# Optimization experiments

Measured on AMD Instinct MI355X. Metric: run time of the kernel, lower is better.

## Reference

```python
import jax, jax.numpy as jnp
import numpy as np

N_QUBITS = 10
DEPTH = 2
FEATURES = 64
HIDDEN = 512
NUM_HIDDEN_LAYERS = 2
BATCH = 32768
DIM = 2 ** N_QUBITS
LOG2PI = float(np.log(2.0 * np.pi))


def _cx_perm(c, t, n):
    # CNOT(control=c, target=t) as a basis permutation (qiskit little-endian bits)
    j = np.arange(2 ** n)
    return j ^ (((j >> c) & 1) << t)

_CX_PERMS = [_cx_perm(q, q + 1, N_QUBITS) for q in range(N_QUBITS - 1)] + [_cx_perm(N_QUBITS - 1, 0, N_QUBITS)]
# Z-expectation sign table: signs[i, j] = +1 if bit i of j is 0 else -1
_SIGNS = np.stack([1.0 - 2.0 * ((np.arange(DIM) >> i) & 1) for i in range(N_QUBITS)]).astype(np.float32)


def _apply_1q(state, gate, q):
    # state: [B, 2^n] complex64; gate: [2,2] (shared) or [B,2,2] (per-sample)
    hi = DIM // (2 ** (q + 1))
    lo = 2 ** q
    s = state.reshape(-1, hi, 2, lo)
    if gate.ndim == 2:
        out = jnp.einsum('ij,bhjl->bhil', gate, s)
    else:
        out = jnp.einsum('bij,bhjl->bhil', gate, s)
    return out.reshape(state.shape)


def _rot_gate(kind, th):
    c = jnp.cos(th / 2).astype(jnp.complex64)
    s = jnp.sin(th / 2).astype(jnp.complex64)
    if kind == 'rx':
        return jnp.stack([jnp.stack([c, -1j * s]), jnp.stack([-1j * s, c])])
    if kind == 'ry':
        return jnp.stack([jnp.stack([c, -s]), jnp.stack([s, c])])
    thc = th.astype(jnp.complex64)
    em = jnp.exp(-0.5j * thc)
    ep = jnp.exp(0.5j * thc)
    z = jnp.zeros((), jnp.complex64)
    return jnp.stack([jnp.stack([em, z]), jnp.stack([z, ep])])


def quantum_expectations(xq, theta):
    # Batched statevector simulation of QuantumLayer circuit. xq: [B, n_qubits]
    B = xq.shape[0]
    state = jnp.zeros((B, DIM), jnp.complex64).at[:, 0].set(1.0)
    # data-encoding RY(2*arctan(x_i)) per qubit (per-sample angle)
    for q in range(N_QUBITS):
        th = 2.0 * jnp.arctan(xq[:, q])
        c = jnp.cos(th / 2).astype(jnp.complex64)
        s = jnp.sin(th / 2).astype(jnp.complex64)
        g = jnp.stack([jnp.stack([c, -s], -1), jnp.stack([s, c], -1)], -2)  # [B,2,2]
        state = _apply_1q(state, g, q)
    idx = 0
    for _ in range(DEPTH):
        for q in range(N_QUBITS):
            state = _apply_1q(state, _rot_gate('rx', theta[idx]), q); idx += 1
            state = _apply_1q(state, _rot_gate('ry', theta[idx]), q); idx += 1
            state = _apply_1q(state, _rot_gate('rz', theta[idx]), q); idx += 1
        for perm in _CX_PERMS:
            state = state[:, perm]
    probs = jnp.abs(state) ** 2  # [B, 2^n]
    return probs @ jnp.asarray(_SIGNS).T  # [B, n_qubits] <Z_i> expectations


def ar_net(x, W_in, b_in, W_h, b_h, W_out, b_out):
    # NOTE: original forward never applies the registered masks -> plain dense MLP
    h = jnp.tanh(x @ W_in.T + b_in)
    for l in range(NUM_HIDDEN_LAYERS):
        h = jnp.tanh(h @ W_h[l].T + b_h[l])
    out = h @ W_out.T + b_out
    shift, log_scale = jnp.split(out, 2, axis=-1)
    return shift, jnp.exp(log_scale)


def setup_inputs() -> dict:
    key = jax.random.key(0)
    ks = jax.random.split(key, 8)

    def lin_w(k, fo, fi):
        b = 1.0 / np.sqrt(fi)
        return jax.random.uniform(k, (fo, fi), jnp.float32, -b, b)

    x = jax.random.normal(ks[0], (BATCH, FEATURES), jnp.float32)
    theta = jax.random.normal(ks[1], (3 * N_QUBITS * DEPTH,), jnp.float32) * 0.01
    W_in = lin_w(ks[2], HIDDEN, FEATURES)
    b_in = jax.random.uniform(ks[3], (HIDDEN,), jnp.float32, -1.0 / np.sqrt(FEATURES), 1.0 / np.sqrt(FEATURES))
    W_h = jnp.stack([lin_w(jax.random.fold_in(ks[4], l), HIDDEN, HIDDEN) for l in range(NUM_HIDDEN_LAYERS)])
    b_h = jax.random.uniform(ks[5], (NUM_HIDDEN_LAYERS, HIDDEN), jnp.float32, -1.0 / np.sqrt(HIDDEN), 1.0 / np.sqrt(HIDDEN))
    W_out = lin_w(ks[6], 2 * FEATURES, HIDDEN)
    b_out = jax.random.uniform(ks[7], (2 * FEATURES,), jnp.float32, -1.0 / np.sqrt(HIDDEN), 1.0 / np.sqrt(HIDDEN))
    return {"x": x, "theta": theta, "W_in": W_in, "b_in": b_in, "W_h": W_h, "b_h": b_h, "W_out": W_out, "b_out": b_out}


def reference(x, theta, W_in, b_in, W_h, b_h, W_out, b_out):
    q = quantum_expectations(x[:, :N_QUBITS], theta)  # [B, n_qubits]
    q = jax.lax.stop_gradient(q)  # torch detaches via torch.tensor(numpy)
    enhanced = jnp.concatenate([q, x[:, N_QUBITS:]], axis=1)  # [B, FEATURES]
    shift, scale = ar_net(enhanced, W_in, b_in, W_h, b_h, W_out, b_out)
    z = (enhanced - shift) / scale
    log_det = -jnp.sum(jnp.log(scale), axis=1)
    log_prob = jnp.sum(-0.5 * z ** 2 - 0.5 * LOG2PI, axis=1) + log_det
    return log_prob
```

## Files before the change

kernel.cpp:

```cpp
#include <hip/hip_runtime.h>
#include <hip/hip_bf16.h>
#include <math.h>


#define N_SAMPLES 32768
#define FEAT 64

typedef unsigned short u16;
typedef __attribute__((ext_vector_type(2))) float f32x2;
typedef __attribute__((ext_vector_type(8))) short bf16x8_t;
typedef __attribute__((ext_vector_type(4))) float f32x4_t;

__device__ __forceinline__ u16 f2bf(float v) {
    __hip_bfloat16 b = __float2bfloat16(v);
    return __builtin_bit_cast(u16, b);
}
__device__ __forceinline__ float bf2f(u16 u) {
    return __bfloat162float(__builtin_bit_cast(__hip_bfloat16, u));
}

__device__ __forceinline__ f32x2 cmul(f32x2 a, f32x2 b) {
    f32x2 r = (f32x2){a.x, a.x} * b;
    f32x2 bs = __builtin_shufflevector(b, b, 1, 0);
    r = (f32x2){-a.y, a.y} * bs + r;
    return r;
}
template<int M>
__device__ __forceinline__ float xexf(float v) {
    if constexpr (M < 32) {
        constexpr int pat = (M << 10) | 0x1f;
        return __uint_as_float(__builtin_amdgcn_ds_swizzle(__float_as_uint(v), pat));
    } else {
        return __shfl_xor(v, 32, 64);
    }
}
template<int M>
__device__ __forceinline__ f32x2 xex2(f32x2 v) {
    return (f32x2){xexf<M>(v.x), xexf<M>(v.y)};
}

template<int Q>
__device__ __forceinline__ void rot_gate(f32x2 (&amp)[16],
                                         f32x2 g00, f32x2 g01, f32x2 g10, f32x2 g11,
                                         int lane) {
    if constexpr (Q < 4) {
        #pragma unroll
        for (int t = 0; t < 16; ++t) {
            if ((t & (1 << Q)) == 0) {
                const int t1 = t | (1 << Q);
                f32x2 a = amp[t], b = amp[t1];
                amp[t]  = cmul(g00, a) + cmul(g01, b);
                amp[t1] = cmul(g10, a) + cmul(g11, b);
            }
        }
    } else {
        constexpr int xm = 1 << (Q - 4);
        const bool hi = (lane >> (Q - 4)) & 1;
        f32x2 ga = hi ? g11 : g00;
        f32x2 gb = hi ? g10 : g01;
        #pragma unroll
        for (int t = 0; t < 16; ++t) {
            f32x2 b = xex2<xm>(amp[t]);
            amp[t] = cmul(ga, amp[t]) + cmul(gb, b);
        }
    }
}

template<int C, int T>
__device__ __forceinline__ void cx_local(f32x2 (&amp)[16]) {
    #pragma unroll
    for (int t = 0; t < 16; ++t) {
        if (((t >> C) & 1) && !((t >> T) & 1)) {
            const int t1 = t | (1 << T);
            f32x2 tmp = amp[t]; amp[t] = amp[t1]; amp[t1] = tmp;
        }
    }
}
__device__ __forceinline__ void cx_3_4(f32x2 (&amp)[16]) {
    #pragma unroll
    for (int t = 0; t < 16; ++t)
        if ((t >> 3) & 1) amp[t] = xex2<1>(amp[t]);
}
template<int CL, int TL>
__device__ __forceinline__ void cx_lane(f32x2 (&amp)[16], int lane) {
    const bool ctrl = (lane >> CL) & 1;
    #pragma unroll
    for (int t = 0; t < 16; ++t) {
        f32x2 v = xex2<(1 << TL)>(amp[t]);
        if (ctrl) amp[t] = v;
    }
}
__device__ __forceinline__ void cx_9_0(f32x2 (&amp)[16], int lane) {
    const bool ctrl = (lane >> 5) & 1;
    #pragma unroll
    for (int t = 0; t < 16; t += 2) {
        f32x2 a = amp[t], b = amp[t + 1];
        amp[t]     = ctrl ? b : a;
        amp[t + 1] = ctrl ? a : b;
    }
}

__global__ __launch_bounds__(256)
void qkernel(const float* __restrict__ x, const float* __restrict__ theta,
             float* __restrict__ enh) {
    __shared__ f32x2 gbuf[20][4];
    const int tid = threadIdx.x;
    if (tid < 20) {
        const int base = tid * 3;
        float s1, c1, s2, c2, sz, cz;
        sincosf(0.5f * theta[base + 0], &s1, &c1);
        sincosf(0.5f * theta[base + 1], &s2, &c2);
        sincosf(0.5f * theta[base + 2], &sz, &cz);
        f32x2 m00 = (f32x2){ c2*c1,  s2*s1};
        f32x2 m01 = (f32x2){-s2*c1, -c2*s1};
        f32x2 m10 = (f32x2){ s2*c1, -c2*s1};
        f32x2 m11 = (f32x2){ c2*c1, -s2*s1};
        f32x2 e0 = (f32x2){cz, -sz}, e1 = (f32x2){cz, sz};
        gbuf[tid][0] = cmul(e0, m00);
        gbuf[tid][1] = cmul(e0, m01);
        gbuf[tid][2] = cmul(e1, m10);
        gbuf[tid][3] = cmul(e1, m11);
    }
    __syncthreads();

    const int lane = tid & 63;
    const int s = blockIdx.x * 4 + (tid >> 6);
    const float xr = x[s * FEAT + lane];

    const float inv = 1.0f / sqrtf(fmaf(xr, xr, 1.0f));
    const float cq = inv, sq = xr * inv;

    float csv[10], snv[10];
    #pragma unroll
    for (int i = 0; i < 10; ++i) {
        csv[i] = __shfl(cq, i, 64);
        snv[i] = __shfl(sq, i, 64);
    }

    float lf = ((lane >> 0) & 1) ? snv[4] : csv[4];
    lf *= ((lane >> 1) & 1) ? snv[5] : csv[5];
    lf *= ((lane >> 2) & 1) ? snv[6] : csv[6];
    lf *= ((lane >> 3) & 1) ? snv[7] : csv[7];
    lf *= ((lane >> 4) & 1) ? snv[8] : csv[8];
    lf *= ((lane >> 5) & 1) ? snv[9] : csv[9];
    float l01[4], l23[4];
    l01[0] = csv[0]*csv[1]; l01[1] = snv[0]*csv[1];
    l01[2] = csv[0]*snv[1]; l01[3] = snv[0]*snv[1];
    l23[0] = csv[2]*csv[3]; l23[1] = snv[2]*csv[3];
    l23[2] = csv[2]*snv[3]; l23[3] = snv[2]*snv[3];

    f32x2 amp[16];
    #pragma unroll
    for (int t = 0; t < 16; ++t)
        amp[t] = (f32x2){lf * l01[t & 3] * l23[(t >> 2) & 3], 0.f};

    #pragma unroll
    for (int l = 0; l < 2; ++l) {
        const f32x2* gl = &gbuf[l * 10][0];
        #define ROT(Q) rot_gate<Q>(amp, gl[Q*4+0], gl[Q*4+1], gl[Q*4+2], gl[Q*4+3], lane);
        ROT(0) ROT(1) ROT(2) ROT(3) ROT(4) ROT(5) ROT(6) ROT(7) ROT(8) ROT(9)
        #undef ROT
        cx_local<0,1>(amp); cx_local<1,2>(amp); cx_local<2,3>(amp);
        cx_3_4(amp);
        cx_lane<0,1>(amp, lane); cx_lane<1,2>(amp, lane); cx_lane<2,3>(amp, lane);
        cx_lane<3,4>(amp, lane); cx_lane<4,5>(amp, lane);
        cx_9_0(amp, lane);
    }

    float p[16];
    #pragma unroll
    for (int t = 0; t < 16; ++t) p[t] = amp[t].x*amp[t].x + amp[t].y*amp[t].y;
    float o[10];
    #pragma unroll
    for (int i = 0; i < 4; ++i) {
        float acc = 0.f;
        #pragma unroll
        for (int t = 0; t < 16; ++t) acc += ((t >> i) & 1) ? -p[t] : p[t];
        o[i] = acc;
    }
    float ptot = 0.f;
    #pragma unroll
    for (int t = 0; t < 16; ++t) ptot += p[t];
    #pragma unroll
    for (int i = 4; i < 10; ++i) o[i] = ((lane >> (i - 4)) & 1) ? -ptot : ptot;
    #pragma unroll
    for (int i = 0; i < 10; ++i) {
        #pragma unroll
        for (int b = 1; b < 64; b <<= 1) o[i] += __shfl_xor(o[i], b, 64);
    }
    float outv = xr;
    #pragma unroll
    for (int i = 0; i < 10; ++i) if (lane == i) outv = o[i];
    enh[s * FEAT + lane] = outv;
}

__global__ __launch_bounds__(256)
void prep(const float* __restrict__ W_in, const float* __restrict__ W_h,
          const float* __restrict__ W_out,
          u16* __restrict__ win_hi, u16* __restrict__ win_lo,
          u16* __restrict__ wh_hi,  u16* __restrict__ wh_lo,
          u16* __restrict__ wout_hi,u16* __restrict__ wout_lo) {
    const int i = blockIdx.x * 256 + threadIdx.x;
    float v; u16 *ph, *pl; int off;
    if (i < 32768)        { v = W_in[i];          ph = win_hi;  pl = win_lo;  off = i; }
    else if (i < 557056)  { off = i - 32768;  v = W_h[off];   ph = wh_hi;   pl = wh_lo;  }
    else                  { off = i - 557056; v = W_out[off]; ph = wout_hi; pl = wout_lo; }
    const u16 hi = f2bf(v);
    const u16 lo = f2bf(v - bf2f(hi));
    ph[off] = hi; pl[off] = lo;
}

__device__ __forceinline__ float fast_tanh(float x) {
    const float e = __expf(2.0f * x);
    return 1.0f - 2.0f * __builtin_amdgcn_rcpf(e + 1.0f);
}

#define MT 4

template<int K, int NT>
__device__ __forceinline__ void gemm_frag(
        const u16* __restrict__ Whi, const u16* __restrict__ Wlo,
        const u16* hHi, const u16* hLo, int lane, int colbase,
        f32x4_t (&acc)[MT][NT]) {
    constexpr int KS = K / 32;
    const int l15 = lane & 15, l4 = lane >> 4, l7 = lane & 7;

    #pragma unroll
    for (int mt = 0; mt < MT; ++mt)
        #pragma unroll
        for (int nt = 0; nt < NT; ++nt) acc[mt][nt] = (f32x4_t)0.f;

    int woff[NT];
    #pragma unroll
    for (int nt = 0; nt < NT; ++nt)
        woff[nt] = (colbase + nt * 16 + l15) * K + l4 * 8;

    bf16x8_t pH[NT], pL[NT], qH[NT], qL[NT];
    #pragma unroll
    for (int nt = 0; nt < NT; ++nt) {
        pH[nt] = *(const bf16x8_t*)&Whi[woff[nt]];
        pL[nt] = *(const bf16x8_t*)&Wlo[woff[nt]];
        qH[nt] = *(const bf16x8_t*)&Whi[woff[nt] + 32];
        qL[nt] = *(const bf16x8_t*)&Wlo[woff[nt] + 32];
    }

    int ks = 0;
    #pragma unroll 1
    for (; ks + 2 < KS; ks += 2) {
        {
            bf16x8_t aH[MT], aL[MT];
            #pragma unroll
            for (int mt = 0; mt < MT; ++mt) {
                const int m = mt * 16 + l15;
                const int off = m * K + (((ks * 4 + l4) ^ (m & 7)) * 8);
                aH[mt] = *(const bf16x8_t*)&hHi[off];
                aL[mt] = *(const bf16x8_t*)&hLo[off];
            }
            #pragma unroll
            for (int nt = 0; nt < NT; ++nt)
                #pragma unroll
                for (int mt = 0; mt < MT; ++mt) {
                    acc[mt][nt] = __builtin_amdgcn_mfma_f32_16x16x32_bf16(aH[mt], pH[nt], acc[mt][nt], 0, 0, 0);
                    acc[mt][nt] = __builtin_amdgcn_mfma_f32_16x16x32_bf16(aH[mt], pL[nt], acc[mt][nt], 0, 0, 0);
                    acc[mt][nt] = __builtin_amdgcn_mfma_f32_16x16x32_bf16(aL[mt], pH[nt], acc[mt][nt], 0, 0, 0);
                }
        }
        #pragma unroll
        for (int nt = 0; nt < NT; ++nt) {
            pH[nt] = *(const bf16x8_t*)&Whi[woff[nt] + (ks + 2) * 32];
            pL[nt] = *(const bf16x8_t*)&Wlo[woff[nt] + (ks + 2) * 32];
        }
        {
            bf16x8_t aH[MT], aL[MT];
            #pragma unroll
            for (int mt = 0; mt < MT; ++mt) {
                const int m = mt * 16 + l15;
                const int off = m * K + ((((ks + 1) * 4 + l4) ^ (m & 7)) * 8);
                aH[mt] = *(const bf16x8_t*)&hHi[off];
                aL[mt] = *(const bf16x8_t*)&hLo[off];
            }
            #pragma unroll
            for (int nt = 0; nt < NT; ++nt)
                #pragma unroll
                for (int mt = 0; mt < MT; ++mt) {
                    acc[mt][nt] = __builtin_amdgcn_mfma_f32_16x16x32_bf16(aH[mt], qH[nt], acc[mt][nt], 0, 0, 0);
                    acc[mt][nt] = __builtin_amdgcn_mfma_f32_16x16x32_bf16(aH[mt], qL[nt], acc[mt][nt], 0, 0, 0);
                    acc[mt][nt] = __builtin_amdgcn_mfma_f32_16x16x32_bf16(aL[mt], qH[nt], acc[mt][nt], 0, 0, 0);
                }
        }
        #pragma unroll
        for (int nt = 0; nt < NT; ++nt) {
            qH[nt] = *(const bf16x8_t*)&Whi[woff[nt] + (ks + 3) * 32];
            qL[nt] = *(const bf16x8_t*)&Wlo[woff[nt] + (ks + 3) * 32];
        }
    }
    {
        bf16x8_t aH[MT], aL[MT];
        #pragma unroll
        for (int mt = 0; mt < MT; ++mt) {
            const int m = mt * 16 + l15;
            const int off = m * K + (((ks * 4 + l4) ^ (m & 7)) * 8);
            aH[mt] = *(const bf16x8_t*)&hHi[off];
            aL[mt] = *(const bf16x8_t*)&hLo[off];
        }
        #pragma unroll
        for (int nt = 0; nt < NT; ++nt)
            #pragma unroll
            for (int mt = 0; mt < MT; ++mt) {
                acc[mt][nt] = __builtin_amdgcn_mfma_f32_16x16x32_bf16(aH[mt], pH[nt], acc[mt][nt], 0, 0, 0);
                acc[mt][nt] = __builtin_amdgcn_mfma_f32_16x16x32_bf16(aH[mt], pL[nt], acc[mt][nt], 0, 0, 0);
                acc[mt][nt] = __builtin_amdgcn_mfma_f32_16x16x32_bf16(aL[mt], pH[nt], acc[mt][nt], 0, 0, 0);
            }
        #pragma unroll
        for (int mt = 0; mt < MT; ++mt) {
            const int m = mt * 16 + l15;
            const int off = m * K + ((((ks + 1) * 4 + l4) ^ (m & 7)) * 8);
            aH[mt] = *(const bf16x8_t*)&hHi[off];
            aL[mt] = *(const bf16x8_t*)&hLo[off];
        }
        #pragma unroll
        for (int nt = 0; nt < NT; ++nt)
            #pragma unroll
            for (int mt = 0; mt < MT; ++mt) {
                acc[mt][nt] = __builtin_amdgcn_mfma_f32_16x16x32_bf16(aH[mt], qH[nt], acc[mt][nt], 0, 0, 0);
                acc[mt][nt] = __builtin_amdgcn_mfma_f32_16x16x32_bf16(aH[mt], qL[nt], acc[mt][nt], 0, 0, 0);
                acc[mt][nt] = __builtin_amdgcn_mfma_f32_16x16x32_bf16(aL[mt], qH[nt], acc[mt][nt], 0, 0, 0);
            }
    }
}

template<int NT>
__device__ __forceinline__ void write_h(
        f32x4_t (&acc)[MT][NT], const float* __restrict__ bias,
        u16* hHi, u16* hLo, int lane, int colbase) {
    const int l15 = lane & 15, l4 = lane >> 4;
    #pragma unroll
    for (int nt = 0; nt < NT; ++nt) {
        const int n = colbase + nt * 16 + l15;
        const float b = bias[n];
        #pragma unroll
        for (int mt = 0; mt < MT; ++mt)
            #pragma unroll
            for (int r = 0; r < 4; ++r) {
                const int m = mt * 16 + l4 * 4 + r;
                const float v = fast_tanh(acc[mt][nt][r] + b);
                const u16 hi = f2bf(v);
                const u16 lo = f2bf(v - bf2f(hi));
                const int blk = (n >> 3) ^ (m & 7);
                const int off = m * 512 + blk * 8 + (n & 7);
                hHi[off] = hi; hLo[off] = lo;
            }
    }
}

__global__ __attribute__((amdgpu_waves_per_eu(2, 2))) __launch_bounds__(512)
void mlpkernel(const float* __restrict__ enh,
               const u16* __restrict__ win_hi, const u16* __restrict__ win_lo,
               const float* __restrict__ b_in,
               const u16* __restrict__ wh_hi,  const u16* __restrict__ wh_lo,
               const float* __restrict__ b_h,
               const u16* __restrict__ wout_hi,const u16* __restrict__ wout_lo,
               const float* __restrict__ b_out,
               float* __restrict__ out) {
    __shared__ u16 hHi[64 * 512];
    __shared__ u16 hLo[64 * 512];
    const int tid = threadIdx.x;
    const int lane = tid & 63, w = tid >> 6;
    const int row0 = blockIdx.x * 64;

    {
        const int r = tid >> 3, c0 = (tid & 7) * 8;
        const float4 v0 = *(const float4*)&enh[(row0 + r) * FEAT + c0];
        const float4 v1 = *(const float4*)&enh[(row0 + r) * FEAT + c0 + 4];
        const float vv[8] = {v0.x, v0.y, v0.z, v0.w, v1.x, v1.y, v1.z, v1.w};
        bf16x8_t vh, vl;
        #pragma unroll
        for (int j = 0; j < 8; ++j) {
            const u16 hi = f2bf(vv[j]);
            const u16 lo = f2bf(vv[j] - bf2f(hi));
            vh[j] = (short)hi; vl[j] = (short)lo;
        }
        const int off = r * 64 + (((c0 >> 3) ^ (r & 7)) * 8);
        *(bf16x8_t*)&hHi[off] = vh;
        *(bf16x8_t*)&hLo[off] = vl;
    }
    __syncthreads();

    f32x4_t acc[MT][4];
    gemm_frag<64, 4>(win_hi, win_lo, hHi, hLo, lane, w * 64, acc);
    __syncthreads();
    write_h<4>(acc, b_in, hHi, hLo, lane, w * 64);
    __syncthreads();
    gemm_frag<512, 4>(wh_hi, wh_lo, hHi, hLo, lane, w * 64, acc);
    __syncthreads();
    write_h<4>(acc, b_h, hHi, hLo, lane, w * 64);
    __syncthreads();
    gemm_frag<512, 4>(wh_hi + 262144, wh_lo + 262144, hHi, hLo, lane, w * 64, acc);
    __syncthreads();
    write_h<4>(acc, b_h + 512, hHi, hLo, lane, w * 64);
    __syncthreads();
    f32x4_t acc2[MT][1];
    gemm_frag<512, 1>(wout_hi, wout_lo, hHi, hLo, lane, w * 16, acc2);
    __syncthreads();

    float* f = (float*)hHi;
    {
        const int l15 = lane & 15, l4 = lane >> 4;
        const int n = w * 16 + l15;
        const float b = b_out[n];
        #pragma unroll
        for (int mt = 0; mt < MT; ++mt)
            #pragma unroll
            for (int r = 0; r < 4; ++r) {
                const int m = mt * 16 + l4 * 4 + r;
                f[m * 128 + n] = acc2[mt][0][r] + b;
            }
    }
    __syncthreads();

    const float HALF_LOG2PI = 0.9189385332046727f;
    #pragma unroll
    for (int rr = 0; rr < 8; ++rr) {
        const int row = w * 8 + rr;
        const float shift = f[row * 128 + lane];
        const float ls    = f[row * 128 + 64 + lane];
        const float e     = enh[(row0 + row) * FEAT + lane];
        const float z = (e - shift) * __expf(-ls);
        float term = fmaf(-0.5f * z, z, -HALF_LOG2PI) - ls;
        #pragma unroll
        for (int b = 1; b < 64; b <<= 1) term += __shfl_xor(term, b, 64);
        if (lane == 0) out[row0 + row] = term;
    }
}

extern "C" void kernel_launch(void* const* d_in, const int* in_sizes, int n_in,
                              void* d_out, int out_size, void* d_ws, size_t ws_size,
                              hipStream_t stream) {
    const float* x     = (const float*)d_in[0];
    const float* theta = (const float*)d_in[1];
    const float* W_in  = (const float*)d_in[2];
    const float* b_in  = (const float*)d_in[3];
    const float* W_h   = (const float*)d_in[4];
    const float* b_h   = (const float*)d_in[5];
    const float* W_out = (const float*)d_in[6];
    const float* b_out = (const float*)d_in[7];
    float* out = (float*)d_out;

    float* enh = (float*)d_ws;
    u16* wbuf = (u16*)((char*)d_ws + (size_t)N_SAMPLES * FEAT * 4);
    u16* win_hi  = wbuf;
    u16* win_lo  = win_hi + 32768;
    u16* wh_hi   = win_lo + 32768;
    u16* wh_lo   = wh_hi + 524288;
    u16* wout_hi = wh_lo + 524288;
    u16* wout_lo = wout_hi + 65536;

    qkernel<<<dim3(N_SAMPLES / 4), dim3(256), 0, stream>>>(x, theta, enh);
    prep<<<dim3(2432), dim3(256), 0, stream>>>(W_in, W_h, W_out,
        win_hi, win_lo, wh_hi, wh_lo, wout_hi, wout_lo);
    mlpkernel<<<dim3(N_SAMPLES / 64), dim3(512), 0, stream>>>(
        enh, win_hi, win_lo, b_in, wh_hi, wh_lo, b_h, wout_hi, wout_lo, b_out, out);
}
```

Before: 438.3 us.

## Fold second-layer CNOT ring into rotated bases and merge quantum/prep kernels

Absorbs the trailing CNOT permutations into the second layer's rotation gates by applying each gate in a transformed basis, using parity-based partner indices and gate selection. The Z expectations are then read from parity sums with lane-dependent sign flips, and the first layer's CNOTs are dropped as separate shuffles. The weight-splitting prep kernel is merged into the quantum kernel launch as extra blocks, removing one launch. The MLP kernel's waves_per_eu lower bound is relaxed from 2 to 1, and the basis-mapping derivation is intricate, so an error would affect correctness.

```diff
diff --git a/kernel.cpp b/kernel.cpp
--- a/kernel.cpp
+++ b/kernel.cpp
@@ -5,6 +5,8 @@
 
 #define N_SAMPLES 32768
 #define FEAT 64
+#define QBLOCKS (N_SAMPLES / 4)
+#define PREPBLOCKS 2432
 
 typedef unsigned short u16;
 typedef __attribute__((ext_vector_type(2))) float f32x2;
@@ -27,11 +29,13 @@
 }
 template<int M>
 __device__ __forceinline__ float xexf(float v) {
-    if constexpr (M < 32) {
+    if constexpr (M == 0) {
+        return v;
+    } else if constexpr (M < 32) {
         constexpr int pat = (M << 10) | 0x1f;
         return __uint_as_float(__builtin_amdgcn_ds_swizzle(__float_as_uint(v), pat));
     } else {
-        return __shfl_xor(v, 32, 64);
+        return __shfl_xor(v, M, 64);
     }
 }
 template<int M>
@@ -66,45 +70,51 @@
     }
 }
 
-template<int C, int T>
-__device__ __forceinline__ void cx_local(f32x2 (&amp)[16]) {
+template<int D, int R>
+__device__ __forceinline__ void rot2(f32x2 (&amp)[16],
+                                     f32x2 g00, f32x2 g01, f32x2 g10, f32x2 g11,
+                                     int lane) {
+    constexpr int DL = D & 15;
+    constexpr int DP = (D >> 4) & 63;
+    constexpr int RL = R & 15;
+    constexpr int RP = (R >> 4) & 63;
+    const bool lp = __popc(lane & RP) & 1;
+    const f32x2 gA0 = lp ? g11 : g00, gB0 = lp ? g10 : g01;
+    const f32x2 gA1 = lp ? g00 : g11, gB1 = lp ? g01 : g10;
+    f32x2 b[16];
+    #pragma unroll
+    for (int t = 0; t < 16; ++t) b[t] = xex2<DP>(amp[t ^ DL]);
     #pragma unroll
     for (int t = 0; t < 16; ++t) {
-        if (((t >> C) & 1) && !((t >> T) & 1)) {
-            const int t1 = t | (1 << T);
-            f32x2 tmp = amp[t]; amp[t] = amp[t1]; amp[t1] = tmp;
-        }
-    }
-}
-__device__ __forceinline__ void cx_3_4(f32x2 (&amp)[16]) {
-    #pragma unroll
-    for (int t = 0; t < 16; ++t)
-        if ((t >> 3) & 1) amp[t] = xex2<1>(amp[t]);
-}
-template<int CL, int TL>
-__device__ __forceinline__ void cx_lane(f32x2 (&amp)[16], int lane) {
-    const bool ctrl = (lane >> CL) & 1;
-    #pragma unroll
-    for (int t = 0; t < 16; ++t) {
-        f32x2 v = xex2<(1 << TL)>(amp[t]);
-        if (ctrl) amp[t] = v;
-    }
-}
-__device__ __forceinline__ void cx_9_0(f32x2 (&amp)[16], int lane) {
-    const bool ctrl = (lane >> 5) & 1;
-    #pragma unroll
-    for (int t = 0; t < 16; t += 2) {
-        f32x2 a = amp[t], b = amp[t + 1];
-        amp[t]     = ctrl ? b : a;
-        amp[t + 1] = ctrl ? a : b;
+        const bool pt = __popc(t & RL) & 1;
+        amp[t] = cmul(pt ? gA1 : gA0, amp[t]) + cmul(pt ? gB1 : gB0, b[t]);
     }
 }
 
 __global__ __launch_bounds__(256)
-void qkernel(const float* __restrict__ x, const float* __restrict__ theta,
-             float* __restrict__ enh) {
+void qprep(const float* __restrict__ x, const float* __restrict__ theta,
+           float* __restrict__ enh,
+           const float* __restrict__ W_in, const float* __restrict__ W_h,
+           const float* __restrict__ W_out,
+           u16* __restrict__ win_hi, u16* __restrict__ win_lo,
+           u16* __restrict__ wh_hi,  u16* __restrict__ wh_lo,
+           u16* __restrict__ wout_hi,u16* __restrict__ wout_lo) {
+    const int tid = threadIdx.x;
+    const int bid = blockIdx.x;
+
+    if (bid >= QBLOCKS) {
+        const int i = (bid - QBLOCKS) * 256 + tid;
+        float v; u16 *ph, *pl; int off;
+        if (i < 32768)        { v = W_in[i];          ph = win_hi;  pl = win_lo;  off = i; }
+        else if (i < 557056)  { off = i - 32768;  v = W_h[off];   ph = wh_hi;   pl = wh_lo;  }
+        else                  { off = i - 557056; v = W_out[off]; ph = wout_hi; pl = wout_lo; }
+        const u16 hi = f2bf(v);
+        const u16 lo = f2bf(v - bf2f(hi));
+        ph[off] = hi; pl[off] = lo;
+        return;
+    }
+
     __shared__ f32x2 gbuf[20][4];
-    const int tid = threadIdx.x;
     if (tid < 20) {
         const int base = tid * 3;
         float s1, c1, s2, c2, sz, cz;
@@ -124,7 +134,7 @@
     __syncthreads();
 
     const int lane = tid & 63;
-    const int s = blockIdx.x * 4 + (tid >> 6);
+    const int s = bid * 4 + (tid >> 6);
     const float xr = x[s * FEAT + lane];
 
     const float inv = 1.0f / sqrtf(fmaf(xr, xr, 1.0f));
@@ -154,35 +164,54 @@
     for (int t = 0; t < 16; ++t)
         amp[t] = (f32x2){lf * l01[t & 3] * l23[(t >> 2) & 3], 0.f};
 
-    #pragma unroll
-    for (int l = 0; l < 2; ++l) {
-        const f32x2* gl = &gbuf[l * 10][0];
-        #define ROT(Q) rot_gate<Q>(amp, gl[Q*4+0], gl[Q*4+1], gl[Q*4+2], gl[Q*4+3], lane);
+    {
+        const f32x2* g1 = &gbuf[0][0];
+        #define ROT(Q) rot_gate<Q>(amp, g1[Q*4+0], g1[Q*4+1], g1[Q*4+2], g1[Q*4+3], lane);
         ROT(0) ROT(1) ROT(2) ROT(3) ROT(4) ROT(5) ROT(6) ROT(7) ROT(8) ROT(9)
         #undef ROT
-        cx_local<0,1>(amp); cx_local<1,2>(amp); cx_local<2,3>(amp);
-        cx_3_4(amp);
-        cx_lane<0,1>(amp, lane); cx_lane<1,2>(amp, lane); cx_lane<2,3>(amp, lane);
-        cx_lane<3,4>(amp, lane); cx_lane<4,5>(amp, lane);
-        cx_9_0(amp, lane);
+    }
+    {
+        const f32x2* g2 = &gbuf[10][0];
+        #define ROT2(Q, D, R) rot2<D, R>(amp, g2[Q*4+0], g2[Q*4+1], g2[Q*4+2], g2[Q*4+3], lane);
+        ROT2(0, 0x003, 0x3FE)
+        ROT2(1, 0x006, 0x003)
+        ROT2(2, 0x00C, 0x007)
+        ROT2(3, 0x018, 0x00F)
+        ROT2(4, 0x030, 0x01F)
+        ROT2(5, 0x060, 0x03F)
+        ROT2(6, 0x0C0, 0x07F)
+        ROT2(7, 0x180, 0x0FF)
+        ROT2(8, 0x300, 0x1FF)
+        ROT2(9, 0x203, 0x3FF)
+        #undef ROT2
     }
 
     float p[16];
     #pragma unroll
     for (int t = 0; t < 16; ++t) p[t] = amp[t].x*amp[t].x + amp[t].y*amp[t].y;
+
+    float S5 = 0.f, SA = 0.f, SB = 0.f, SD = 0.f;
+    #pragma unroll
+    for (int t = 0; t < 16; ++t) {
+        S5 += (__popc(t & 0x5) & 1) ? -p[t] : p[t];
+        SA += (__popc(t & 0xA) & 1) ? -p[t] : p[t];
+        SB += (__popc(t & 0xB) & 1) ? -p[t] : p[t];
+        SD += (__popc(t & 0xD) & 1) ? -p[t] : p[t];
+    }
     float o[10];
-    #pragma unroll
-    for (int i = 0; i < 4; ++i) {
-        float acc = 0.f;
-        #pragma unroll
-        for (int t = 0; t < 16; ++t) acc += ((t >> i) & 1) ? -p[t] : p[t];
-        o[i] = acc;
-    }
-    float ptot = 0.f;
-    #pragma unroll
-    for (int t = 0; t < 16; ++t) ptot += p[t];
-    #pragma unroll
-    for (int i = 4; i < 10; ++i) o[i] = ((lane >> (i - 4)) & 1) ? -ptot : ptot;
+    o[0] = SB; o[1] = SD; o[2] = SA; o[3] = S5; o[4] = SA;
+    o[5] = S5; o[6] = SA; o[7] = S5; o[8] = SA; o[9] = S5;
+    if (__popc(lane & 0x2A) & 1) o[0] = -o[0];
+    if (__popc(lane & 0x3F) & 1) o[1] = -o[1];
+    if (__popc(lane & 0x3F) & 1) o[2] = -o[2];
+    if (__popc(lane & 0x3F) & 1) o[3] = -o[3];
+    if (__popc(lane & 0x3E) & 1) o[4] = -o[4];
+    if (__popc(lane & 0x3D) & 1) o[5] = -o[5];
+    if (__popc(lane & 0x3A) & 1) o[6] = -o[6];
+    if (__popc(lane & 0x35) & 1) o[7] = -o[7];
+    if (__popc(lane & 0x2A) & 1) o[8] = -o[8];
+    if (__popc(lane & 0x15) & 1) o[9] = -o[9];
+
     #pragma unroll
     for (int i = 0; i < 10; ++i) {
         #pragma unroll
@@ -192,22 +221,6 @@
     #pragma unroll
     for (int i = 0; i < 10; ++i) if (lane == i) outv = o[i];
     enh[s * FEAT + lane] = outv;
-}
-
-__global__ __launch_bounds__(256)
-void prep(const float* __restrict__ W_in, const float* __restrict__ W_h,
-          const float* __restrict__ W_out,
-          u16* __restrict__ win_hi, u16* __restrict__ win_lo,
-          u16* __restrict__ wh_hi,  u16* __restrict__ wh_lo,
-          u16* __restrict__ wout_hi,u16* __restrict__ wout_lo) {
-    const int i = blockIdx.x * 256 + threadIdx.x;
-    float v; u16 *ph, *pl; int off;
-    if (i < 32768)        { v = W_in[i];          ph = win_hi;  pl = win_lo;  off = i; }
-    else if (i < 557056)  { off = i - 32768;  v = W_h[off];   ph = wh_hi;   pl = wh_lo;  }
-    else                  { off = i - 557056; v = W_out[off]; ph = wout_hi; pl = wout_lo; }
-    const u16 hi = f2bf(v);
-    const u16 lo = f2bf(v - bf2f(hi));
-    ph[off] = hi; pl[off] = lo;
 }
 
 __device__ __forceinline__ float fast_tanh(float x) {
@@ -353,7 +366,7 @@
     }
 }
 
-__global__ __attribute__((amdgpu_waves_per_eu(2, 2))) __launch_bounds__(512)
+__global__ __attribute__((amdgpu_waves_per_eu(1, 2))) __launch_bounds__(512)
 void mlpkernel(const float* __restrict__ enh,
                const u16* __restrict__ win_hi, const u16* __restrict__ win_lo,
                const float* __restrict__ b_in,
@@ -455,8 +468,8 @@
     u16* wout_hi = wh_lo + 524288;
     u16* wout_lo = wout_hi + 65536;
 
-    qkernel<<<dim3(N_SAMPLES / 4), dim3(256), 0, stream>>>(x, theta, enh);
-    prep<<<dim3(2432), dim3(256), 0, stream>>>(W_in, W_h, W_out,
+    qprep<<<dim3(QBLOCKS + PREPBLOCKS), dim3(256), 0, stream>>>(
+        x, theta, enh, W_in, W_h, W_out,
         win_hi, win_lo, wh_hi, wh_lo, wout_hi, wout_lo);
     mlpkernel<<<dim3(N_SAMPLES / 64), dim3(512), 0, stream>>>(
         enh, win_hi, win_lo, b_in, wh_hi, wh_lo, b_h, wout_hi, wout_lo, b_out, out);
```

New measurement: 427.0 us. 2.6% less time.
